# Optimization experiments

Hardware: AMD Instinct MI355X
Metric: run time of the kernel (lower is better)

The kernel has to match this reference:

```python
import jax, jax.numpy as jnp
import numpy as np

SEQ, D = 4096, 1024  # vector_size == dimension == 1024


def setup_inputs() -> dict:
    key = jax.random.key(0)
    ks = jax.random.split(key, 7)
    s = 1.0 / np.sqrt(D)
    return {
        "X": jax.random.normal(ks[0], (SEQ, D), dtype=jnp.float32),
        "Wq": jax.random.normal(ks[1], (D, D), dtype=jnp.float32) * s,
        "bq": jax.random.normal(ks[2], (D,), dtype=jnp.float32) * s,
        "Wk": jax.random.normal(ks[3], (D, D), dtype=jnp.float32) * s,
        "bk": jax.random.normal(ks[4], (D,), dtype=jnp.float32) * s,
        "Wv": jax.random.normal(ks[5], (D, D), dtype=jnp.float32) * s,
        "bv": jax.random.normal(ks[6], (D,), dtype=jnp.float32) * s,
    }


def reference(X, Wq, bq, Wk, bk, Wv, bv):
    # Batched QKV projections (nn.Linear: x @ W^T + b), replacing the per-vector loop.
    Q = X @ Wq.T + bq            # [S, D]
    K = X @ Wk.T + bk            # [S, D]
    V = X @ Wv.T + bv            # [S, D]
    scale = 1.0 / jnp.sqrt(jnp.asarray(D, dtype=X.dtype))
    scores = (Q @ K.T) * scale   # [S, S]
    attn = jax.nn.softmax(scores, axis=1)
    return attn @ V              # [S, D]
```

## Files before the change

### kernel.cpp

```cpp
#include <hip/hip_runtime.h>
#include <hip/hip_bf16.h>
#include <stdint.h>


typedef __bf16 bf16_t;
typedef __bf16 bf16x4 __attribute__((ext_vector_type(4)));
typedef __bf16 bf16x8 __attribute__((ext_vector_type(8)));
typedef float f32x4 __attribute__((ext_vector_type(4)));

#define AS1 __attribute__((address_space(1)))
#define AS3 __attribute__((address_space(3)))

__device__ __forceinline__ void async_ld16(const void* g, void* l) {
  __builtin_amdgcn_global_load_lds((AS1 void*)g, (AS3 void*)l, 16, 0, 0);
}

template <int MODE, int BN, int BK>
__global__ __launch_bounds__(256, 2) void gemm_k(
    const bf16_t* __restrict__ A, const bf16_t* __restrict__ B, const int ld,
    const int Klen,
    bf16_t* __restrict__ o0, bf16_t* __restrict__ o1, bf16_t* __restrict__ o2,
    const float* __restrict__ b0, const float* __restrict__ b1,
    const float* __restrict__ b2, float* __restrict__ fout,
    float* __restrict__ rowsum) {
  constexpr int NF = BN / 32;
  constexpr int KS = BK / 32;
  constexpr int CH = BK / 8;
  constexpr int RS = 256 / CH;
  __shared__ bf16_t As[128 * BK];
  __shared__ bf16_t Bs[BN * BK];

  const int t = threadIdx.x;
  const int lane = t & 63;
  const int wave = t >> 6;
  const int wm = wave >> 1;
  const int wn = wave & 1;
  const int q = lane >> 4;
  const int l16 = lane & 15;
  const int wnoff = wn * (BN / 2);

  int m0, n0, k0, zz = 0;
  if constexpr (MODE == 1) {
    const int bid = blockIdx.y * 32 + blockIdx.x;
    const int xcd = bid & 7, sl = bid >> 3;
    m0 = ((xcd >> 2) * 16 + (sl >> 3)) * 128;
    n0 = ((xcd & 3) * 8 + (sl & 7)) * BN;
    k0 = 0;
  } else if constexpr (MODE == 2) {
    const int lin = blockIdx.x;
    const int xcd = lin & 7;
    const int s = lin >> 3;
    zz = xcd >> 1;
    const int mt = (xcd & 1) * 16 + (s >> 3);
    const int nt = s & 7;
    m0 = mt * 128;
    n0 = nt * 128;
    k0 = zz * Klen;
  } else {
    n0 = blockIdx.x * BN;
    m0 = blockIdx.y * 128;
    k0 = blockIdx.z * Klen;
  }

  const f32x4 zero4 = {0.f, 0.f, 0.f, 0.f};
  f32x4 acc[4][NF];
#pragma unroll
  for (int i = 0; i < 4; ++i)
#pragma unroll
    for (int j = 0; j < NF; ++j) acc[i][j] = zero4;

  const int srow = t / CH;
  const int schunk =
      (t % CH) ^ ((BK == 32) ? ((srow >> 1) & 3) : (srow & 7));
  const bf16_t* Ab = A + (size_t)(m0 + srow) * ld + k0 + schunk * 8;
  const bf16_t* Bb = B + (size_t)(n0 + srow) * ld + k0 + schunk * 8;
  bf16_t* Asl = As + t * 8;
  bf16_t* Bsl = Bs + t * 8;

  const int xf = (BK == 32) ? ((l16 >> 1) & 3) : (l16 & 7);
  const int ar = wm * 64 + l16;
  const int br = wnoff + l16;

  for (int kt = 0; kt < Klen; kt += BK) {
#pragma unroll
    for (int rr = 0; rr < 128 / RS; ++rr)
      async_ld16(Ab + kt + (size_t)(rr * RS) * ld, Asl + rr * RS * BK);
#pragma unroll
    for (int rr = 0; rr < BN / RS; ++rr)
      async_ld16(Bb + kt + (size_t)(rr * RS) * ld, Bsl + rr * RS * BK);
    __syncthreads();

#pragma unroll
    for (int s = 0; s < KS; ++s) {
      bf16x8 fa[4], fb[NF];
#pragma unroll
      for (int im = 0; im < 4; ++im)
        fa[im] = *(const bf16x8*)(As + (ar + im * 16) * BK +
                                  (((s * 4 + q) ^ xf) * 8));
#pragma unroll
      for (int j = 0; j < NF; ++j)
        fb[j] = *(const bf16x8*)(Bs + (br + j * 16) * BK +
                                 (((s * 4 + q) ^ xf) * 8));
#pragma unroll
      for (int im = 0; im < 4; ++im)
#pragma unroll
        for (int j = 0; j < NF; ++j)
          acc[im][j] = __builtin_amdgcn_mfma_f32_16x16x32_bf16(
              fa[im], fb[j], acc[im][j], 0, 0, 0);
    }
    __syncthreads();
  }

  const int mBase = m0 + wm * 64 + q * 4;

  if constexpr (MODE == 0) {
    const int sel = n0 >> 10;
    const int nl0 = (n0 & 1023) + wnoff + l16;
    const float* bias = (sel == 0) ? b0 : ((sel == 1) ? b1 : b2);
    const float sc = (sel == 0) ? 0.03125f : 1.0f;
#pragma unroll
    for (int j = 0; j < NF; ++j) {
      const int nl = nl0 + j * 16;
      const float bb = bias[nl];
#pragma unroll
      for (int im = 0; im < 4; ++im) {
        const int mr = mBase + im * 16;
        if (sel < 2) {
          bf16_t* dst = (sel == 0) ? o0 : o1;
#pragma unroll
          for (int r = 0; r < 4; ++r)
            dst[(size_t)(mr + r) * 1024 + nl] =
                (bf16_t)((acc[im][j][r] + bb) * sc);
        } else {
          bf16x4 v;
#pragma unroll
          for (int r = 0; r < 4; ++r) v[r] = (bf16_t)(acc[im][j][r] + bb);
          *(bf16x4*)(o2 + (size_t)nl * 4096 + mr) = v;
        }
      }
    }
  } else if constexpr (MODE == 1) {
    float ps[4][4];
#pragma unroll
    for (int im = 0; im < 4; ++im)
#pragma unroll
      for (int r = 0; r < 4; ++r) ps[im][r] = 0.f;
#pragma unroll
    for (int j = 0; j < NF; ++j) {
      const int n = n0 + wnoff + j * 16 + l16;
#pragma unroll
      for (int im = 0; im < 4; ++im) {
        const int mr = mBase + im * 16;
#pragma unroll
        for (int r = 0; r < 4; ++r) {
          const float e = __expf(acc[im][j][r]);
          ps[im][r] += e;
          o0[(size_t)(mr + r) * 4096 + n] = (bf16_t)e;
        }
      }
    }
#pragma unroll
    for (int im = 0; im < 4; ++im)
#pragma unroll
      for (int r = 0; r < 4; ++r) {
        float v = ps[im][r];
        v += __shfl_xor(v, 1);
        v += __shfl_xor(v, 2);
        v += __shfl_xor(v, 4);
        v += __shfl_xor(v, 8);
        ps[im][r] = v;
      }
    if (l16 == 0) {
#pragma unroll
      for (int im = 0; im < 4; ++im)
#pragma unroll
        for (int r = 0; r < 4; ++r)
          atomicAdd(rowsum + mBase + im * 16 + r, ps[im][r]);
    }
  } else {
    float inv[4][4];
#pragma unroll
    for (int im = 0; im < 4; ++im)
#pragma unroll
      for (int r = 0; r < 4; ++r)
        inv[im][r] = 1.0f / rowsum[mBase + im * 16 + r];
    if (zz < 3) {
      bf16_t* pp = (zz == 0) ? o0 : ((zz == 1) ? o1 : o2);
#pragma unroll
      for (int im = 0; im < 4; ++im) {
        const int mr = mBase + im * 16;
#pragma unroll
        for (int j = 0; j < NF; ++j) {
          const int n = n0 + wnoff + j * 16 + l16;
#pragma unroll
          for (int r = 0; r < 4; ++r)
            pp[(size_t)(mr + r) * 1024 + n] =
                (bf16_t)(acc[im][j][r] * inv[im][r]);
        }
      }
    } else {
#pragma unroll
      for (int im = 0; im < 4; ++im) {
        const int mr = mBase + im * 16;
#pragma unroll
        for (int j = 0; j < NF; ++j) {
          const int n = n0 + wnoff + j * 16 + l16;
#pragma unroll
          for (int r = 0; r < 4; ++r)
            fout[(size_t)(mr + r) * 1024 + n] = acc[im][j][r] * inv[im][r];
        }
      }
    }
  }
}

__global__ __launch_bounds__(256) void cvt_all(
    const float* __restrict__ X, const float* __restrict__ Wq,
    const float* __restrict__ Wk, const float* __restrict__ Wv,
    bf16_t* __restrict__ Xb, bf16_t* __restrict__ Wb,
    float* __restrict__ rowsum) {
  int i = blockIdx.x * 256 + threadIdx.x;
  if (i >= 1835008) {
    rowsum[i - 1835008] = 0.f;
    return;
  }
  const float* src;
  bf16_t* dst;
  int off;
  if (i < 1048576) {
    src = X; dst = Xb; off = i;
  } else {
    const int w = i - 1048576;
    const int sel = w >> 18;
    off = w & 0x3FFFF;
    src = (sel == 0) ? Wq : ((sel == 1) ? Wk : Wv);
    dst = Wb + (size_t)sel * (1024 * 1024);
  }
  const float4 v = ((const float4*)src)[off];
  bf16x4 o;
  o[0] = (bf16_t)v.x; o[1] = (bf16_t)v.y; o[2] = (bf16_t)v.z; o[3] = (bf16_t)v.w;
  ((bf16x4*)dst)[off] = o;
}

__global__ __launch_bounds__(256) void reduce_out(
    const bf16_t* __restrict__ p0, const bf16_t* __restrict__ p1,
    const bf16_t* __restrict__ p2, float* __restrict__ out) {
  const int i = blockIdx.x * 256 + threadIdx.x;
  const bf16x8 a = ((const bf16x8*)p0)[i];
  const bf16x8 b = ((const bf16x8*)p1)[i];
  const bf16x8 c = ((const bf16x8*)p2)[i];
  float4 lo = ((const float4*)out)[2 * i];
  float4 hi = ((const float4*)out)[2 * i + 1];
  lo.x += (float)a[0] + (float)b[0] + (float)c[0];
  lo.y += (float)a[1] + (float)b[1] + (float)c[1];
  lo.z += (float)a[2] + (float)b[2] + (float)c[2];
  lo.w += (float)a[3] + (float)b[3] + (float)c[3];
  hi.x += (float)a[4] + (float)b[4] + (float)c[4];
  hi.y += (float)a[5] + (float)b[5] + (float)c[5];
  hi.z += (float)a[6] + (float)b[6] + (float)c[6];
  hi.w += (float)a[7] + (float)b[7] + (float)c[7];
  ((float4*)out)[2 * i] = lo;
  ((float4*)out)[2 * i + 1] = hi;
}

extern "C" void kernel_launch(void* const* d_in, const int* in_sizes, int n_in,
                              void* d_out, int out_size, void* d_ws,
                              size_t ws_size, hipStream_t stream) {
  const int S = 4096, D = 1024;
  const float* X  = (const float*)d_in[0];
  const float* Wq = (const float*)d_in[1];
  const float* bq = (const float*)d_in[2];
  const float* Wk = (const float*)d_in[3];
  const float* bk = (const float*)d_in[4];
  const float* Wv = (const float*)d_in[5];
  const float* bv = (const float*)d_in[6];
  float* out = (float*)d_out;

  bf16_t* Xb = (bf16_t*)d_ws;
  bf16_t* Wb = Xb + (size_t)S * D;
  bf16_t* Qb = Wb + (size_t)3 * D * D;
  bf16_t* Kb = Qb + (size_t)S * D;
  bf16_t* Vt = Kb + (size_t)S * D;
  bf16_t* Sc = Vt + (size_t)D * S;
  float* rowsum = (float*)(Sc + (size_t)S * S);

  cvt_all<<<7184, 256, 0, stream>>>(X, Wq, Wk, Wv, Xb, Wb, rowsum);

  gemm_k<0, 128, 64><<<dim3(3 * D / 128, S / 128), 256, 0, stream>>>(
      Xb, Wb, D, D, Qb, Kb, Vt, bq, bk, bv, nullptr, nullptr);
  gemm_k<1, 128, 64><<<dim3(S / 128, S / 128), 256, 0, stream>>>(
      Qb, Kb, D, D, Sc, nullptr, nullptr, nullptr, nullptr, nullptr, nullptr,
      rowsum);
  gemm_k<2, 128, 64><<<1024, 256, 0, stream>>>(
      Sc, Vt, S, S / 4, Xb, Qb, Kb, nullptr, nullptr, nullptr, out, rowsum);
  reduce_out<<<S * D / 8 / 256, 256, 0, stream>>>(Xb, Qb, Kb, out);
}
```

Measured before the change: 206.9 us.

## Fuse all stages into one persistent cooperative kernel with grid syncs

Replaces the five separate launches (convert, QKV projection, scores, PV, reduce) with one cooperative persistent kernel of 512 blocks that loops over tiles per stage and separates stages with grid.sync. This removes launch overhead and inter-kernel gaps. The cost is fixed occupancy: the QKV stage has 768 tiles on 512 blocks, so some blocks run two tiles while others idle, and each stage ends in a grid-wide barrier. Falls back to the separate kernels if occupancy is below 2 blocks per CU.

```diff
diff --git a/kernel.cpp b/kernel.cpp
--- a/kernel.cpp
+++ b/kernel.cpp
@@ -1,4 +1,5 @@
 #include <hip/hip_runtime.h>
+#include <hip/hip_cooperative_groups.h>
 #include <hip/hip_bf16.h>
 #include <stdint.h>
 
@@ -8,6 +9,8 @@
 typedef __bf16 bf16x8 __attribute__((ext_vector_type(8)));
 typedef float f32x4 __attribute__((ext_vector_type(4)));
 
+namespace cg = cooperative_groups;
+
 #define AS1 __attribute__((address_space(1)))
 #define AS3 __attribute__((address_space(3)))
 
@@ -15,22 +18,24 @@
   __builtin_amdgcn_global_load_lds((AS1 void*)g, (AS3 void*)l, 16, 0, 0);
 }
 
-template <int MODE, int BN, int BK>
-__global__ __launch_bounds__(256, 2) void gemm_k(
-    const bf16_t* __restrict__ A, const bf16_t* __restrict__ B, const int ld,
-    const int Klen,
-    bf16_t* __restrict__ o0, bf16_t* __restrict__ o1, bf16_t* __restrict__ o2,
-    const float* __restrict__ b0, const float* __restrict__ b1,
-    const float* __restrict__ b2, float* __restrict__ fout,
-    float* __restrict__ rowsum) {
+template <int MODE>
+__device__ void gemm_core(bf16_t* As, bf16_t* Bs, const int t, const int m0,
+                          const int n0, const int k0, const int zz,
+                          const bf16_t* __restrict__ A,
+                          const bf16_t* __restrict__ B, const int ld,
+                          const int Klen, bf16_t* __restrict__ o0,
+                          bf16_t* __restrict__ o1, bf16_t* __restrict__ o2,
+                          const float* __restrict__ b0,
+                          const float* __restrict__ b1,
+                          const float* __restrict__ b2,
+                          float* __restrict__ fout,
+                          float* __restrict__ rowsum) {
+  constexpr int BN = 128, BK = 64;
   constexpr int NF = BN / 32;
   constexpr int KS = BK / 32;
   constexpr int CH = BK / 8;
   constexpr int RS = 256 / CH;
-  __shared__ bf16_t As[128 * BK];
-  __shared__ bf16_t Bs[BN * BK];
-
-  const int t = threadIdx.x;
+
   const int lane = t & 63;
   const int wave = t >> 6;
   const int wm = wave >> 1;
@@ -39,29 +44,6 @@
   const int l16 = lane & 15;
   const int wnoff = wn * (BN / 2);
 
-  int m0, n0, k0, zz = 0;
-  if constexpr (MODE == 1) {
-    const int bid = blockIdx.y * 32 + blockIdx.x;
-    const int xcd = bid & 7, sl = bid >> 3;
-    m0 = ((xcd >> 2) * 16 + (sl >> 3)) * 128;
-    n0 = ((xcd & 3) * 8 + (sl & 7)) * BN;
-    k0 = 0;
-  } else if constexpr (MODE == 2) {
-    const int lin = blockIdx.x;
-    const int xcd = lin & 7;
-    const int s = lin >> 3;
-    zz = xcd >> 1;
-    const int mt = (xcd & 1) * 16 + (s >> 3);
-    const int nt = s & 7;
-    m0 = mt * 128;
-    n0 = nt * 128;
-    k0 = zz * Klen;
-  } else {
-    n0 = blockIdx.x * BN;
-    m0 = blockIdx.y * 128;
-    k0 = blockIdx.z * Klen;
-  }
-
   const f32x4 zero4 = {0.f, 0.f, 0.f, 0.f};
   f32x4 acc[4][NF];
 #pragma unroll
@@ -70,14 +52,13 @@
     for (int j = 0; j < NF; ++j) acc[i][j] = zero4;
 
   const int srow = t / CH;
-  const int schunk =
-      (t % CH) ^ ((BK == 32) ? ((srow >> 1) & 3) : (srow & 7));
+  const int schunk = (t % CH) ^ (srow & 7);
   const bf16_t* Ab = A + (size_t)(m0 + srow) * ld + k0 + schunk * 8;
   const bf16_t* Bb = B + (size_t)(n0 + srow) * ld + k0 + schunk * 8;
   bf16_t* Asl = As + t * 8;
   bf16_t* Bsl = Bs + t * 8;
 
-  const int xf = (BK == 32) ? ((l16 >> 1) & 3) : (l16 & 7);
+  const int xf = l16 & 7;
   const int ar = wm * 64 + l16;
   const int br = wnoff + l16;
 
@@ -212,6 +193,125 @@
       }
     }
   }
+}
+
+__global__ __launch_bounds__(256, 2) void fused_attn(
+    const float* __restrict__ X, const float* __restrict__ Wq,
+    const float* __restrict__ bq, const float* __restrict__ Wk,
+    const float* __restrict__ bk, const float* __restrict__ Wv,
+    const float* __restrict__ bv, float* __restrict__ out,
+    bf16_t* __restrict__ Xb, bf16_t* __restrict__ Wb,
+    bf16_t* __restrict__ Qb, bf16_t* __restrict__ Kb,
+    bf16_t* __restrict__ Vt, bf16_t* __restrict__ Sc,
+    float* __restrict__ rowsum) {
+  __shared__ bf16_t As[128 * 64];
+  __shared__ bf16_t Bs[128 * 64];
+  cg::grid_group grid = cg::this_grid();
+  const int bid = blockIdx.x;
+  const int t = threadIdx.x;
+
+  for (int u = bid; u < 7184; u += 512) {
+    const int i = u * 256 + t;
+    if (i >= 1835008) {
+      rowsum[i - 1835008] = 0.f;
+    } else {
+      const float* src;
+      bf16_t* dst;
+      int off;
+      if (i < 1048576) {
+        src = X; dst = Xb; off = i;
+      } else {
+        const int w = i - 1048576;
+        const int sel = w >> 18;
+        off = w & 0x3FFFF;
+        src = (sel == 0) ? Wq : ((sel == 1) ? Wk : Wv);
+        dst = Wb + (size_t)sel * (1024 * 1024);
+      }
+      const float4 v = ((const float4*)src)[off];
+      bf16x4 o;
+      o[0] = (bf16_t)v.x; o[1] = (bf16_t)v.y;
+      o[2] = (bf16_t)v.z; o[3] = (bf16_t)v.w;
+      ((bf16x4*)dst)[off] = o;
+    }
+  }
+  grid.sync();
+
+  for (int v = bid; v < 768; v += 512) {
+    const int n0 = (v % 24) * 128;
+    const int m0 = (v / 24) * 128;
+    gemm_core<0>(As, Bs, t, m0, n0, 0, 0, Xb, Wb, 1024, 1024, Qb, Kb, Vt, bq,
+                 bk, bv, nullptr, nullptr);
+  }
+  grid.sync();
+
+  for (int v = bid; v < 1024; v += 512) {
+    const int xcd = v & 7, sl = v >> 3;
+    const int m0 = ((xcd >> 2) * 16 + (sl >> 3)) * 128;
+    const int n0 = ((xcd & 3) * 8 + (sl & 7)) * 128;
+    gemm_core<1>(As, Bs, t, m0, n0, 0, 0, Qb, Kb, 1024, 1024, Sc, nullptr,
+                 nullptr, nullptr, nullptr, nullptr, nullptr, rowsum);
+  }
+  grid.sync();
+
+  for (int v = bid; v < 1024; v += 512) {
+    const int xcd = v & 7, s = v >> 3;
+    const int zz = xcd >> 1;
+    const int mt = (xcd & 1) * 16 + (s >> 3);
+    const int nt = s & 7;
+    gemm_core<2>(As, Bs, t, mt * 128, nt * 128, zz * 1024, zz, Sc, Vt, 4096,
+                 1024, Xb, Qb, Kb, nullptr, nullptr, nullptr, out, rowsum);
+  }
+  grid.sync();
+
+  for (int u = bid; u < 2048; u += 512) {
+    const int i = u * 256 + t;
+    const bf16x8 a = ((const bf16x8*)Xb)[i];
+    const bf16x8 b = ((const bf16x8*)Qb)[i];
+    const bf16x8 c = ((const bf16x8*)Kb)[i];
+    float4 lo = ((const float4*)out)[2 * i];
+    float4 hi = ((const float4*)out)[2 * i + 1];
+    lo.x += (float)a[0] + (float)b[0] + (float)c[0];
+    lo.y += (float)a[1] + (float)b[1] + (float)c[1];
+    lo.z += (float)a[2] + (float)b[2] + (float)c[2];
+    lo.w += (float)a[3] + (float)b[3] + (float)c[3];
+    hi.x += (float)a[4] + (float)b[4] + (float)c[4];
+    hi.y += (float)a[5] + (float)b[5] + (float)c[5];
+    hi.z += (float)a[6] + (float)b[6] + (float)c[6];
+    hi.w += (float)a[7] + (float)b[7] + (float)c[7];
+    ((float4*)out)[2 * i] = lo;
+    ((float4*)out)[2 * i + 1] = hi;
+  }
+}
+
+template <int MODE>
+__global__ __launch_bounds__(256, 2) void gemm_sep(
+    const bf16_t* __restrict__ A, const bf16_t* __restrict__ B, const int ld,
+    const int Klen,
+    bf16_t* __restrict__ o0, bf16_t* __restrict__ o1, bf16_t* __restrict__ o2,
+    const float* __restrict__ b0, const float* __restrict__ b1,
+    const float* __restrict__ b2, float* __restrict__ fout,
+    float* __restrict__ rowsum) {
+  __shared__ bf16_t As[128 * 64];
+  __shared__ bf16_t Bs[128 * 64];
+  int m0, n0, k0 = 0, zz = 0;
+  if constexpr (MODE == 1) {
+    const int bid = blockIdx.y * 32 + blockIdx.x;
+    const int xcd = bid & 7, sl = bid >> 3;
+    m0 = ((xcd >> 2) * 16 + (sl >> 3)) * 128;
+    n0 = ((xcd & 3) * 8 + (sl & 7)) * 128;
+  } else if constexpr (MODE == 2) {
+    const int lin = blockIdx.x;
+    const int xcd = lin & 7, s = lin >> 3;
+    zz = xcd >> 1;
+    m0 = ((xcd & 1) * 16 + (s >> 3)) * 128;
+    n0 = (s & 7) * 128;
+    k0 = zz * Klen;
+  } else {
+    n0 = blockIdx.x * 128;
+    m0 = blockIdx.y * 128;
+  }
+  gemm_core<MODE>(As, Bs, threadIdx.x, m0, n0, k0, zz, A, B, ld, Klen, o0, o1,
+                  o2, b0, b1, b2, fout, rowsum);
 }
 
 __global__ __launch_bounds__(256) void cvt_all(
@@ -284,14 +384,25 @@
   bf16_t* Sc = Vt + (size_t)D * S;
   float* rowsum = (float*)(Sc + (size_t)S * S);
 
-  cvt_all<<<7184, 256, 0, stream>>>(X, Wq, Wk, Wv, Xb, Wb, rowsum);
-
-  gemm_k<0, 128, 64><<<dim3(3 * D / 128, S / 128), 256, 0, stream>>>(
-      Xb, Wb, D, D, Qb, Kb, Vt, bq, bk, bv, nullptr, nullptr);
-  gemm_k<1, 128, 64><<<dim3(S / 128, S / 128), 256, 0, stream>>>(
-      Qb, Kb, D, D, Sc, nullptr, nullptr, nullptr, nullptr, nullptr, nullptr,
-      rowsum);
-  gemm_k<2, 128, 64><<<1024, 256, 0, stream>>>(
-      Sc, Vt, S, S / 4, Xb, Qb, Kb, nullptr, nullptr, nullptr, out, rowsum);
-  reduce_out<<<S * D / 8 / 256, 256, 0, stream>>>(Xb, Qb, Kb, out);
-}
+  int occ = 0;
+  hipError_t qerr =
+      hipOccupancyMaxActiveBlocksPerMultiprocessor(&occ, fused_attn, 256, 0);
+  const bool useCoop = (qerr == hipSuccess) && (occ >= 2);
+
+  if (useCoop) {
+    void* args[] = {&X, &Wq, &bq, &Wk, &bk, &Wv, &bv, &out,
+                    &Xb, &Wb, &Qb, &Kb, &Vt, &Sc, &rowsum};
+    hipLaunchCooperativeKernel(reinterpret_cast<void*>(fused_attn), dim3(512),
+                               dim3(256), args, 0, stream);
+  } else {
+    cvt_all<<<7184, 256, 0, stream>>>(X, Wq, Wk, Wv, Xb, Wb, rowsum);
+    gemm_sep<0><<<dim3(24, 32), 256, 0, stream>>>(
+        Xb, Wb, D, D, Qb, Kb, Vt, bq, bk, bv, nullptr, nullptr);
+    gemm_sep<1><<<dim3(32, 32), 256, 0, stream>>>(
+        Qb, Kb, D, D, Sc, nullptr, nullptr, nullptr, nullptr, nullptr, nullptr,
+        rowsum);
+    gemm_sep<2><<<1024, 256, 0, stream>>>(
+        Sc, Vt, S, S / 4, Xb, Qb, Kb, nullptr, nullptr, nullptr, out, rowsum);
+    reduce_out<<<S * D / 8 / 256, 256, 0, stream>>>(Xb, Qb, Kb, out);
+  }
+}
```

New measurement: 236.0 us. 1.14x slower.
